# Kernel tuning notes

Hardware: AMD Instinct MI355X
Metric: run time of the kernel (lower is better)

The kernel has to match this reference:

```python
import jax, jax.numpy as jnp
import numpy as np

MUL = 128                  # multiplicity of each irrep slot in in1 / out
Z = 100000                 # batch (e.g. number of edges)
L = [0, 1]                 # l of irrep slot i; dims are 2l+1 -> [1, 3]
INSTR = [(0, 0, 0), (0, 1, 1), (1, 0, 1), (1, 1, 0)]  # parity-allowed 'uvw' paths


def _w3j_np(l1, l2, l3):
    """Real-basis Wigner-3j (e3nn convention) for l <= 1."""
    if (l1, l2, l3) == (0, 0, 0):
        return np.ones((1, 1, 1))
    e = np.eye(3) / np.sqrt(3.0)
    if (l1, l2, l3) == (1, 1, 0):
        return e[:, :, None]
    if (l1, l2, l3) == (0, 1, 1):
        return e[None, :, :]
    if (l1, l2, l3) == (1, 0, 1):
        return e[:, None, :]
    raise ValueError((l1, l2, l3))


# fan-in per output slot for component-normalized path weights
FAN_IN = {0: 0, 1: 0}
for (_i1, _i2, _io) in INSTR:
    FAN_IN[_io] += MUL * 1  # mul_in1 * mul_in2 for 'uvw'

WEIGHT_NUMEL = len(INSTR) * MUL * 1 * MUL  # 65536


def setup_inputs() -> dict:
    key = jax.random.key(0)
    k1, k2, k3 = jax.random.split(key, 3)
    x1 = jax.random.normal(k1, (Z, MUL * 1 + MUL * 3), jnp.float32)   # 128x0e + 128x1o
    x2 = jax.random.normal(k2, (Z, 1 + 3), jnp.float32)               # 1x0e + 1x1o
    weights = jax.random.normal(k3, (WEIGHT_NUMEL,), jnp.float32)     # shared 'uvw' weights
    return {"x1": x1, "x2": x2, "weights": weights}


def _tensor_product(x1, x2, weights):
    z = x1.shape[0]
    # split flat features into (mul, 2l+1) segments
    x1s = [x1[:, :MUL].reshape(z, MUL, 1), x1[:, MUL:].reshape(z, MUL, 3)]
    x2s = [x2[:, :1].reshape(z, 1, 1), x2[:, 1:].reshape(z, 1, 3)]
    outs = [jnp.zeros((z, MUL, 1), x1.dtype), jnp.zeros((z, MUL, 3), x1.dtype)]
    off = 0
    for (i1, i2, io) in INSTR:
        nw = MUL * 1 * MUL
        w = weights[off:off + nw].reshape(MUL, 1, MUL)  # (u, v, w)
        off += nw
        C = jnp.asarray(_w3j_np(L[i1], L[i2], L[io]), x1.dtype)
        pw = jnp.asarray(np.sqrt(2 * L[io] + 1.0) / np.sqrt(FAN_IN[io]), x1.dtype)
        # segmented CG contraction: small (i,j,k) dims, large z,u,w dims
        tmp = jnp.einsum('zui,zvj,ijk->zuvk', x1s[i1], x2s[i2], C)
        outs[io] = outs[io] + pw * jnp.einsum('zuvk,uvw->zwk', tmp, w)
    return jnp.concatenate([o.reshape(z, -1) for o in outs], axis=1)


def reference(x1, x2, weights):
    return _tensor_product(x1, x2, weights)
```

## Files before the change

### kernel.cpp

```cpp
#include <hip/hip_runtime.h>


#define Z_TOTAL   100000
#define BM        32
#define NTILES_Z  (Z_TOTAL / BM)
#define GRID      512
#define THREADS   512

using bf16x8 = __attribute__((ext_vector_type(8))) __bf16;
using f32x4  = __attribute__((ext_vector_type(4))) float;
using u16x8  = __attribute__((ext_vector_type(8))) unsigned short;

__device__ __forceinline__ unsigned short f2bf(float f) {
    unsigned int u = __builtin_bit_cast(unsigned int, f);
    u += 0x7fffu + ((u >> 16) & 1u);
    return (unsigned short)(u >> 16);
}

__device__ __forceinline__ int lds_idx(int row, int chunk) {
    return row * 256 + ((chunk ^ (row & 7)) << 3);
}

__global__ __launch_bounds__(THREADS, 4)
void tp_kernel(const float* __restrict__ x1, const float* __restrict__ x2,
               const float* __restrict__ wts, float* __restrict__ out)
{
    __shared__ __align__(16) unsigned short lds[128 * 256];

    const int t    = threadIdx.x;
    const int lane = t & 63;
    const int wv   = t >> 6;
    const int m16  = lane & 15;
    const int q    = lane >> 4;

    const float S16 = 0.0625f;
    const float S48 = 0.0625f * 0.57735026918962576f;
    bf16x8 Bf[2][8];
    {
        const int n = wv * 16 + m16;
        #pragma unroll
        for (int mat = 0; mat < 2; ++mat) {
            #pragma unroll
            for (int kt = 0; kt < 8; ++kt) {
                u16x8 bb;
                #pragma unroll
                for (int j = 0; j < 8; ++j) {
                    const int k = kt * 32 + q * 8 + j;
                    float v;
                    if (mat == 0) {
                        v = (k < 128) ? wts[k * 128 + n] * S16
                                      : wts[49152 + (k - 128) * 128 + n] * S48;
                    } else {
                        v = (k < 128) ? wts[16384 + k * 128 + n] * S16
                                      : wts[32768 + (k - 128) * 128 + n] * S16;
                    }
                    bb[j] = f2bf(v);
                }
                Bf[mat][kt] = __builtin_bit_cast(bf16x8, bb);
            }
        }
    }

    const int zl = t >> 4;
    const int ug = t & 15;
    const int u0 = ug * 8;

    for (int tile = blockIdx.x; tile < NTILES_Z; tile += gridDim.x) {
        const int z0 = tile * BM;
        const float* xr = x1 + (size_t)(z0 + zl) * 512;

        __syncthreads();
        {
            const float4 b4 = *(const float4*)(x2 + (size_t)(z0 + zl) * 4);
            const float b0 = b4.x, b1x = b4.y, b1y = b4.z, b1z = b4.w;

            const float4 a0a = *(const float4*)(xr + u0);
            const float4 a0b = *(const float4*)(xr + u0 + 4);
            const float a0[8] = {a0a.x, a0a.y, a0a.z, a0a.w,
                                 a0b.x, a0b.y, a0b.z, a0b.w};
            u16x8 pk;
            #pragma unroll
            for (int i = 0; i < 8; ++i) pk[i] = f2bf(b0 * a0[i]);
            *(u16x8*)&lds[lds_idx(zl, ug)] = pk;
            #pragma unroll
            for (int i = 0; i < 8; ++i) pk[i] = f2bf(b1x * a0[i]);
            *(u16x8*)&lds[lds_idx(32 + zl, ug)] = pk;
            #pragma unroll
            for (int i = 0; i < 8; ++i) pk[i] = f2bf(b1y * a0[i]);
            *(u16x8*)&lds[lds_idx(64 + zl, ug)] = pk;
            #pragma unroll
            for (int i = 0; i < 8; ++i) pk[i] = f2bf(b1z * a0[i]);
            *(u16x8*)&lds[lds_idx(96 + zl, ug)] = pk;

            float a1[24];
            #pragma unroll
            for (int i = 0; i < 6; ++i) {
                const float4 v = *(const float4*)(xr + 128 + u0 * 3 + i * 4);
                a1[i*4+0] = v.x; a1[i*4+1] = v.y; a1[i*4+2] = v.z; a1[i*4+3] = v.w;
            }
            #pragma unroll
            for (int i = 0; i < 8; ++i)
                pk[i] = f2bf(a1[3*i]*b1x + a1[3*i+1]*b1y + a1[3*i+2]*b1z);
            *(u16x8*)&lds[lds_idx(zl, 16 + ug)] = pk;
            #pragma unroll
            for (int i = 0; i < 8; ++i) pk[i] = f2bf(b0 * a1[3*i + 0]);
            *(u16x8*)&lds[lds_idx(32 + zl, 16 + ug)] = pk;
            #pragma unroll
            for (int i = 0; i < 8; ++i) pk[i] = f2bf(b0 * a1[3*i + 1]);
            *(u16x8*)&lds[lds_idx(64 + zl, 16 + ug)] = pk;
            #pragma unroll
            for (int i = 0; i < 8; ++i) pk[i] = f2bf(b0 * a1[3*i + 2]);
            *(u16x8*)&lds[lds_idx(96 + zl, 16 + ug)] = pk;
        }
        __syncthreads();

        const int n = wv * 16 + m16;
        #pragma unroll
        for (int mt = 0; mt < 8; ++mt) {
            const int isV1 = (mt >= 2) ? 1 : 0;
            const int k3 = isV1 ? ((mt - 2) >> 1) : 0;
            const int zt = isV1 ? ((mt - 2) & 1) : 0;
            const int rbase = isV1 ? (32 + k3 * 32 + zt * 16) : (mt * 16);
            const int r = rbase + m16;
            f32x4 acc = {0.f, 0.f, 0.f, 0.f};
            #pragma unroll
            for (int kt = 0; kt < 8; ++kt) {
                const bf16x8 a = __builtin_bit_cast(bf16x8,
                    *(const u16x8*)&lds[lds_idx(r, kt * 4 + q)]);
                acc = __builtin_amdgcn_mfma_f32_16x16x32_bf16(a, Bf[isV1][kt], acc, 0, 0, 0);
            }
            if (!isV1) {
                #pragma unroll
                for (int reg = 0; reg < 4; ++reg) {
                    const int z = z0 + mt * 16 + q * 4 + reg;
                    out[(size_t)z * 512 + n] = acc[reg];
                }
            } else {
                #pragma unroll
                for (int reg = 0; reg < 4; ++reg) {
                    const int z = z0 + zt * 16 + q * 4 + reg;
                    out[(size_t)z * 512 + 128 + n * 3 + k3] = acc[reg];
                }
            }
        }
    }
}

extern "C" void kernel_launch(void* const* d_in, const int* in_sizes, int n_in,
                              void* d_out, int out_size, void* d_ws, size_t ws_size,
                              hipStream_t stream) {
    (void)in_sizes; (void)n_in; (void)d_ws; (void)ws_size; (void)out_size;
    const float* x1  = (const float*)d_in[0];
    const float* x2  = (const float*)d_in[1];
    const float* wts = (const float*)d_in[2];
    float* out = (float*)d_out;
    tp_kernel<<<dim3(GRID), dim3(THREADS), 0, stream>>>(x1, x2, wts, out);
}
```

Before: 380.3 us.

## Prefetch next tile's inputs into registers and group vector-output MFMAs for packed stores

The global loads of x1/x2 for the next tile are now issued right after the LDS staging barrier, so they overlap the current tile's MFMA work instead of stalling at the start of each tile. The l=1 output path now runs the three k-components' MFMA chains together and writes each (z,n) triple as one contiguous 12-byte store, replacing three strided scalar stores. This adds roughly 40 live registers for the prefetch and three accumulators, which may pressure occupancy under launch_bounds(512,4).

```diff
diff --git a/kernel.cpp b/kernel.cpp
--- a/kernel.cpp
+++ b/kernel.cpp
@@ -10,6 +10,8 @@
 using bf16x8 = __attribute__((ext_vector_type(8))) __bf16;
 using f32x4  = __attribute__((ext_vector_type(4))) float;
 using u16x8  = __attribute__((ext_vector_type(8))) unsigned short;
+
+struct f3 { float x, y, z; };
 
 __device__ __forceinline__ unsigned short f2bf(float f) {
     unsigned int u = __builtin_bit_cast(unsigned int, f);
@@ -64,20 +66,35 @@
     const int zl = t >> 4;
     const int ug = t & 15;
     const int u0 = ug * 8;
+    const int n  = wv * 16 + m16;
 
-    for (int tile = blockIdx.x; tile < NTILES_Z; tile += gridDim.x) {
+    float4 a0a, a0b, a1v[6], b4;
+    {
+        const int z = blockIdx.x * BM + zl;
+        const float* xr = x1 + (size_t)z * 512;
+        a0a = *(const float4*)(xr + u0);
+        a0b = *(const float4*)(xr + u0 + 4);
+        #pragma unroll
+        for (int i = 0; i < 6; ++i)
+            a1v[i] = *(const float4*)(xr + 128 + u0 * 3 + i * 4);
+        b4 = *(const float4*)(x2 + (size_t)z * 4);
+    }
+
+    for (int tile = blockIdx.x; tile < NTILES_Z; tile += GRID) {
         const int z0 = tile * BM;
-        const float* xr = x1 + (size_t)(z0 + zl) * 512;
+        const int nxt = tile + GRID;
 
         __syncthreads();
         {
-            const float4 b4 = *(const float4*)(x2 + (size_t)(z0 + zl) * 4);
             const float b0 = b4.x, b1x = b4.y, b1y = b4.z, b1z = b4.w;
-
-            const float4 a0a = *(const float4*)(xr + u0);
-            const float4 a0b = *(const float4*)(xr + u0 + 4);
             const float a0[8] = {a0a.x, a0a.y, a0a.z, a0a.w,
                                  a0b.x, a0b.y, a0b.z, a0b.w};
+            float a1[24];
+            #pragma unroll
+            for (int i = 0; i < 6; ++i) {
+                a1[i*4+0] = a1v[i].x; a1[i*4+1] = a1v[i].y;
+                a1[i*4+2] = a1v[i].z; a1[i*4+3] = a1v[i].w;
+            }
             u16x8 pk;
             #pragma unroll
             for (int i = 0; i < 8; ++i) pk[i] = f2bf(b0 * a0[i]);
@@ -91,13 +108,6 @@
             #pragma unroll
             for (int i = 0; i < 8; ++i) pk[i] = f2bf(b1z * a0[i]);
             *(u16x8*)&lds[lds_idx(96 + zl, ug)] = pk;
-
-            float a1[24];
-            #pragma unroll
-            for (int i = 0; i < 6; ++i) {
-                const float4 v = *(const float4*)(xr + 128 + u0 * 3 + i * 4);
-                a1[i*4+0] = v.x; a1[i*4+1] = v.y; a1[i*4+2] = v.z; a1[i*4+3] = v.w;
-            }
             #pragma unroll
             for (int i = 0; i < 8; ++i)
                 pk[i] = f2bf(a1[3*i]*b1x + a1[3*i+1]*b1y + a1[3*i+2]*b1z);
@@ -114,33 +124,52 @@
         }
         __syncthreads();
 
-        const int n = wv * 16 + m16;
+        if (nxt < NTILES_Z) {
+            const int z = nxt * BM + zl;
+            const float* xr = x1 + (size_t)z * 512;
+            a0a = *(const float4*)(xr + u0);
+            a0b = *(const float4*)(xr + u0 + 4);
+            #pragma unroll
+            for (int i = 0; i < 6; ++i)
+                a1v[i] = *(const float4*)(xr + 128 + u0 * 3 + i * 4);
+            b4 = *(const float4*)(x2 + (size_t)z * 4);
+        }
+
         #pragma unroll
-        for (int mt = 0; mt < 8; ++mt) {
-            const int isV1 = (mt >= 2) ? 1 : 0;
-            const int k3 = isV1 ? ((mt - 2) >> 1) : 0;
-            const int zt = isV1 ? ((mt - 2) & 1) : 0;
-            const int rbase = isV1 ? (32 + k3 * 32 + zt * 16) : (mt * 16);
-            const int r = rbase + m16;
+        for (int mt = 0; mt < 2; ++mt) {
             f32x4 acc = {0.f, 0.f, 0.f, 0.f};
+            const int r = mt * 16 + m16;
             #pragma unroll
             for (int kt = 0; kt < 8; ++kt) {
                 const bf16x8 a = __builtin_bit_cast(bf16x8,
                     *(const u16x8*)&lds[lds_idx(r, kt * 4 + q)]);
-                acc = __builtin_amdgcn_mfma_f32_16x16x32_bf16(a, Bf[isV1][kt], acc, 0, 0, 0);
+                acc = __builtin_amdgcn_mfma_f32_16x16x32_bf16(a, Bf[0][kt], acc, 0, 0, 0);
             }
-            if (!isV1) {
-                #pragma unroll
-                for (int reg = 0; reg < 4; ++reg) {
-                    const int z = z0 + mt * 16 + q * 4 + reg;
-                    out[(size_t)z * 512 + n] = acc[reg];
-                }
-            } else {
-                #pragma unroll
-                for (int reg = 0; reg < 4; ++reg) {
-                    const int z = z0 + zt * 16 + q * 4 + reg;
-                    out[(size_t)z * 512 + 128 + n * 3 + k3] = acc[reg];
-                }
+            #pragma unroll
+            for (int reg = 0; reg < 4; ++reg) {
+                const int z = z0 + mt * 16 + q * 4 + reg;
+                out[(size_t)z * 512 + n] = acc[reg];
+            }
+        }
+        #pragma unroll
+        for (int zt = 0; zt < 2; ++zt) {
+            f32x4 ax = {0.f,0.f,0.f,0.f}, ay = {0.f,0.f,0.f,0.f}, az = {0.f,0.f,0.f,0.f};
+            const int rx = 32 + zt * 16 + m16;
+            #pragma unroll
+            for (int kt = 0; kt < 8; ++kt) {
+                const int c = kt * 4 + q;
+                const bf16x8 vx = __builtin_bit_cast(bf16x8, *(const u16x8*)&lds[lds_idx(rx,      c)]);
+                const bf16x8 vy = __builtin_bit_cast(bf16x8, *(const u16x8*)&lds[lds_idx(rx + 32, c)]);
+                const bf16x8 vz = __builtin_bit_cast(bf16x8, *(const u16x8*)&lds[lds_idx(rx + 64, c)]);
+                ax = __builtin_amdgcn_mfma_f32_16x16x32_bf16(vx, Bf[1][kt], ax, 0, 0, 0);
+                ay = __builtin_amdgcn_mfma_f32_16x16x32_bf16(vy, Bf[1][kt], ay, 0, 0, 0);
+                az = __builtin_amdgcn_mfma_f32_16x16x32_bf16(vz, Bf[1][kt], az, 0, 0, 0);
+            }
+            #pragma unroll
+            for (int reg = 0; reg < 4; ++reg) {
+                const int z = z0 + zt * 16 + q * 4 + reg;
+                f3 v; v.x = ax[reg]; v.y = ay[reg]; v.z = az[reg];
+                *(f3*)&out[(size_t)z * 512 + 128 + n * 3] = v;
             }
         }
     }
```

Result: slower. 436.8 us (+14.8%).
